# Performance work log

Hardware: AMD Instinct MI355X
Metric: run time of the kernel (lower is better)

The kernel has to match this reference:

```python
import jax, jax.numpy as jnp
import numpy as np
import math

GRID_SIZE = 5
ORDER = 3
TAU = 0.1            # HuxleyRD tau (constructor default)
Q_SCALE = 64 / 2.0   # SaturatedQuantizer levels=64


def make_grid():
    h = 2.0 / GRID_SIZE
    # knots: arange(-order, grid_size+order+1)*h - 1  -> 12 values, shared by all in_features
    return jnp.arange(-ORDER, GRID_SIZE + ORDER + 1, dtype=jnp.float32) * h - 1.0


def b_splines(x, grid):
    # x: [b, in] -> bases: [b, in, GRID_SIZE+ORDER] via vectorized Cox-de Boor
    xg = x[..., None]
    g = grid  # [12], identical per feature so plain broadcasting suffices
    bases = ((xg >= g[:-1]) & (xg < g[1:])).astype(x.dtype)  # [b, in, 11]
    for p in range(1, ORDER + 1):
        t_i, t_ip = g[:-1 - p], g[p:-1]
        term1 = (xg - t_i) / (t_ip - t_i + 1e-8) * bases[..., :-1]
        t_i1, t_ip1 = g[1:-p], g[p + 1:]
        term2 = (t_ip1 - xg) / (t_ip1 - t_i1 + 1e-8) * bases[..., 1:]
        bases = term1 + term2
    return bases  # [b, in, 8]


def kan_layer(x, base_w, spline_w, grid):
    base = x @ base_w.T
    basis = b_splines(x, grid)
    # SaturatedQuantizer forward (round to levels); STE expressed via stop_gradient
    qw = spline_w + jax.lax.stop_gradient(jnp.round(spline_w * Q_SCALE) / Q_SCALE - spline_w)
    return base + jnp.einsum('bic,oic->bo', basis, qw)


def trig_unfolding(u, gcve_pressure, chirality, tau_decay):
    # u: [b, n]
    tr_c = jnp.sum(u * u, axis=-1)                                   # [b]
    uf_abs = jnp.abs(jnp.fft.rfft(u, axis=-1))                       # [b, n//2+1]
    det_pas = jnp.var(uf_abs, axis=-1, ddof=1) + 1e-6                # torch.var is unbiased
    denom = 2.0 * jnp.sqrt(det_pas) ** 3 + 1e-8
    cos_3phi = jnp.clip((3.0 * gcve_pressure - tr_c / tau_decay) / denom, -0.999, 0.999)
    phi = jnp.arccos(cos_3phi) / 3.0                                 # [b]
    lam_min = jnp.min(uf_abs, axis=-1)                               # [b]
    amp = 2.0 * jnp.sqrt(lam_min / 3.0 + 1e-8)                       # [b]
    ks = jnp.arange(3, dtype=u.dtype)                                # branch indices 0,1,2
    cos_terms = jnp.cos(phi[None, :] + 2.0 * jnp.pi * ks[:, None] / 3.0)   # [3, b]
    shifts = jnp.exp(-jnp.abs(chirality)[None, :] * ks[:, None])           # [3, b]
    coef = amp[None, :] * cos_terms * shifts                                # [3, b]
    branches = coef[:, :, None] * u[None, :, :]                             # [3, b, n]
    energies = jnp.linalg.norm(branches, axis=-1)                           # [3, b]
    best_k = jnp.argmax(energies, axis=0)                                   # [b]
    mask = (best_k[None, :] == jnp.arange(3)[:, None]).astype(u.dtype)      # [3, b]
    return jnp.sum(branches * mask[:, :, None], axis=0)


def huxley_rd(u, spectral_gate, kernel, a, gamma, tau_decay, soliton_velocity,
              gcve_pressure, chirality):
    N = u.shape[-1]
    # HarmonicWaveDecomposition: spectral sigmoid gate split
    uf = jnp.fft.rfft(u, axis=-1)
    gate = jax.nn.sigmoid(spectral_gate)
    u_erg = jnp.fft.irfft(uf * gate, n=N, axis=-1)
    u_ne = jnp.fft.irfft(uf * (1.0 - gate), n=N, axis=-1)
    # ergodic: cubic reaction + 3-tap diffusion conv (padding=1, cross-correlation)
    reaction = u_erg * (u_erg - a) * (1.0 - u_erg)
    up = jnp.pad(u_erg, ((0, 0), (1, 1)))
    diffusion = kernel[0] * up[:, :-2] + kernel[1] * up[:, 1:-1] + kernel[2] * up[:, 2:]
    u_erg_next = u_erg + TAU * (reaction + gamma * diffusion)
    # non-ergodic: spectral phase shift (soliton translation)
    nef = jnp.fft.rfft(u_ne, axis=-1)
    k_idx = jnp.arange(nef.shape[-1], dtype=jnp.float32)
    phase = jnp.exp(-1j * 2.0 * jnp.pi * k_idx * soliton_velocity / N)
    u_ne_shift = jnp.fft.irfft(nef * phase, n=N, axis=-1)
    u_ne_unf = trig_unfolding(u_ne_shift, gcve_pressure, chirality, tau_decay)
    s = u_erg_next + u_ne_unf
    return jax.nn.sigmoid(s) * s  # SiLU-style fusion


def setup_inputs() -> dict:
    key = jax.random.key(0)
    ks = jax.random.split(key, 12)
    B, NIN, W, NOUT = 4096, 512, 1024, 1024
    return {
        'c': jax.random.uniform(ks[0], (B, NIN), jnp.float32, -1.0, 1.0),
        'base_w0': jax.random.normal(ks[1], (W, NIN), jnp.float32) * (1.0 / np.sqrt(NIN)),
        'spline_w0': jax.random.normal(ks[2], (W, NIN, 8), jnp.float32) * 0.1,
        'base_w1': jax.random.normal(ks[3], (W, W), jnp.float32) * (1.0 / np.sqrt(W)),
        'spline_w1': jax.random.normal(ks[4], (W, W, 8), jnp.float32) * 0.1,
        'base_w2': jax.random.normal(ks[5], (NOUT, W), jnp.float32) * (1.0 / np.sqrt(W)),
        'spline_w2': jax.random.normal(ks[6], (NOUT, W, 8), jnp.float32) * 0.1,
        'spectral_gate': jnp.ones((NOUT // 2 + 1,), jnp.float32),
        'diffusion_kernel': jnp.asarray([0.1, -0.2, 0.1], jnp.float32),
        'a_param': jnp.asarray(0.1, jnp.float32),
        'gamma': jnp.asarray(1.0, jnp.float32),
        'tau_decay': jnp.asarray(0.1, jnp.float32),
        'soliton_velocity': jnp.asarray(0.25, jnp.float32),
        'gcve_pressure': jax.random.uniform(ks[7], (B,), jnp.float32),
        'chirality': jax.random.normal(ks[8], (B,), jnp.float32),
    }


def reference(c, base_w0, spline_w0, base_w1, spline_w1, base_w2, spline_w2,
              spectral_gate, diffusion_kernel, a_param, gamma, tau_decay,
              soliton_velocity, gcve_pressure, chirality):
    grid = make_grid()
    x = kan_layer(c, base_w0, spline_w0, grid)
    x = kan_layer(x, base_w1, spline_w1, grid)
    x = kan_layer(x, base_w2, spline_w2, grid)
    return huxley_rd(x, spectral_gate, diffusion_kernel, a_param, gamma,
                     tau_decay, soliton_velocity, gcve_pressure, chirality)
```

## Files before the change

### kernel.cpp

```cpp
#include <hip/hip_runtime.h>
#include <math.h>

typedef _Float16 f16;
typedef _Float16 f16x8 __attribute__((ext_vector_type(8)));
typedef float f32x4 __attribute__((ext_vector_type(4)));

__global__ __launch_bounds__(256) void expand_sum_a(
    const float* __restrict__ src, size_t plane, int Sin,
    f16* __restrict__ Aexp, int KIN, int shift)
{
    int idx = blockIdx.x * 256 + threadIdx.x;
    int i = idx & (KIN - 1);
    int b = idx >> shift;
    float x = 0.0f;
    for (int s = 0; s < Sin; ++s) x += src[(size_t)s * plane + idx];

    float xs = (x + 2.2f) * 2.5f;
    float fj = floorf(xs);
    int jj = (int)fj;
    float t = xs - fj;
    float t2 = t * t, t3 = t2 * t;
    float omt = 1.0f - t;
    float p0 = omt * omt * omt * (1.0f / 6.0f);
    float p1 = (3.0f * t3 - 6.0f * t2 + 4.0f) * (1.0f / 6.0f);
    float p2 = (-3.0f * t3 + 3.0f * t2 + 3.0f * t + 1.0f) * (1.0f / 6.0f);
    float p3 = t3 * (1.0f / 6.0f);

    union { f16 h[8]; uint4 v; } hi, lo;
    bool inr = (jj >= 0 && jj <= 10);
    #pragma unroll
    for (int cc = 0; cc < 8; ++cc) {
        int d = cc - (jj - 3);
        float v = 0.0f;
        if (inr) {
            if (d == 0) v = p0; else if (d == 1) v = p1;
            else if (d == 2) v = p2; else if (d == 3) v = p3;
        }
        f16 h = (f16)v;
        hi.h[cc] = h;
        lo.h[cc] = (f16)(v - (float)h);
    }
    size_t KEXP = (size_t)KIN * 19;
    f16* row = Aexp + (size_t)b * KEXP;
    *(uint4*)(row + (size_t)i * 8) = hi.v;
    *(uint4*)(row + (size_t)KIN * 8 + (size_t)i * 8) = lo.v;
    f16 xh = (f16)x;
    f16 xl = (f16)(x - (float)xh);
    int K16 = KIN * 16;
    row[K16 + i] = xh;
    row[K16 + KIN + i] = xh;
    row[K16 + 2 * KIN + i] = xl;
}

__global__ __launch_bounds__(256) void prep_b(
    const float* __restrict__ BW, const float* __restrict__ SW,
    f16* __restrict__ Bexp, int KIN, int shift)
{
    int idx = blockIdx.x * 256 + threadIdx.x;
    int i = idx & (KIN - 1);
    int o = idx >> shift;
    const float* sp = SW + ((size_t)o * KIN + i) * 8;
    union { f16 h[8]; uint4 v; } pk;
    #pragma unroll
    for (int cc = 0; cc < 8; ++cc)
        pk.h[cc] = (f16)(rintf(sp[cc] * 32.0f) * 0.03125f);
    size_t KEXP = (size_t)KIN * 19;
    f16* row = Bexp + (size_t)o * KEXP;
    *(uint4*)(row + (size_t)i * 8) = pk.v;
    *(uint4*)(row + (size_t)KIN * 8 + (size_t)i * 8) = pk.v;
    float w = BW[(size_t)o * KIN + i];
    f16 wh = (f16)w;
    f16 wl = (f16)(w - (float)wh);
    int K16 = KIN * 16;
    row[K16 + i] = wh;
    row[K16 + KIN + i] = wl;
    row[K16 + 2 * KIN + i] = wh;
}

__global__ __launch_bounds__(512, 2) void gemm_mfma(
    const f16* __restrict__ A, const f16* __restrict__ Bm,
    float* __restrict__ C, int Kfull, int Kc, size_t plane, int N)
{
    __shared__ __align__(16) f16 As[4][8192];
    __shared__ __align__(16) f16 Bs[4][8192];

    const int tid = threadIdx.x;
    const int wave = tid >> 6, lane = tid & 63;

    const int nwg = gridDim.x * gridDim.y * gridDim.z;
    const int b = blockIdx.x + gridDim.x * (blockIdx.y + gridDim.y * blockIdx.z);
    const int q = nwg >> 3;
    const int L = (b & 7) * q + (b >> 3);
    const int lx = L % gridDim.x;
    const int rest = L / gridDim.x;
    const int ly = rest % gridDim.y;
    const int lz = rest / gridDim.y;

    const int m0 = ly * 256, n0 = lx * 256;
    const int kb = lz * Kc;
    int kcl = Kfull - kb; if (kcl > Kc) kcl = Kc;
    const int NT = kcl >> 5;

    const int kc_src = (lane & 3) ^ ((lane >> 3) & 3);
    const f16* gb[4];
    int isA_[4], coff[4];
    #pragma unroll
    for (int j = 0; j < 4; ++j) {
        int cch = wave * 4 + j;
        int a = (cch < 16);
        int c8 = a ? cch : (cch - 16);
        int row0 = (a ? m0 : n0) + c8 * 16 + (lane >> 2);
        gb[j] = (a ? A : Bm) + (size_t)row0 * Kfull + kb + kc_src * 8;
        isA_[j] = a;
        coff[j] = c8 * 512;
    }

    f32x4 acc[8][4];
    #pragma unroll
    for (int i = 0; i < 8; ++i)
        #pragma unroll
        for (int j = 0; j < 4; ++j)
            acc[i][j] = (f32x4){0.f, 0.f, 0.f, 0.f};

    #pragma unroll
    for (int s = 0; s < 3; ++s) {
        if (s < NT) {
            int k0 = s << 5;
            #pragma unroll
            for (int j = 0; j < 4; ++j) {
                f16* dp = isA_[j] ? &As[s][coff[j]] : &Bs[s][coff[j]];
                __builtin_amdgcn_global_load_lds(
                    (const __attribute__((address_space(1))) unsigned int*)(gb[j] + k0),
                    (__attribute__((address_space(3))) unsigned int*)dp, 16, 0, 0);
            }
        }
    }
    if (NT >= 3)      asm volatile("s_waitcnt vmcnt(8)" ::: "memory");
    else if (NT == 2) asm volatile("s_waitcnt vmcnt(4)" ::: "memory");
    else              asm volatile("s_waitcnt vmcnt(0)" ::: "memory");
    __builtin_amdgcn_s_barrier();
    asm volatile("" ::: "memory");

    const int lr = lane & 15;
    const int ko = (((lane >> 4) ^ ((lr >> 1) & 3)) & 3) * 8;
    const int wm = (wave & 1) * 128, wn = (wave >> 1) * 64;

    for (int t = 0; t < NT; ++t) {
        const int st = t & 3;
        const int ns = (t + 3) & 3;
        const bool pf = (t + 3 < NT);
        const int kn = (t + 3) << 5;
        const int rem = NT - 1 - t;

        f16x8 af[4], bf[4], ag[4];
        #pragma unroll
        for (int i = 0; i < 4; ++i)
            af[i] = *(const f16x8*)&As[st][(wm + i * 16 + lr) * 32 + ko];
        #pragma unroll
        for (int j = 0; j < 4; ++j)
            bf[j] = *(const f16x8*)&Bs[st][(wn + j * 16 + lr) * 32 + ko];
        if (pf) {
            #pragma unroll
            for (int j = 0; j < 2; ++j) {
                f16* dp = isA_[j] ? &As[ns][coff[j]] : &Bs[ns][coff[j]];
                __builtin_amdgcn_global_load_lds(
                    (const __attribute__((address_space(1))) unsigned int*)(gb[j] + kn),
                    (__attribute__((address_space(3))) unsigned int*)dp, 16, 0, 0);
            }
        }
        #pragma unroll
        for (int i = 0; i < 4; ++i)
            ag[i] = *(const f16x8*)&As[st][(wm + 64 + i * 16 + lr) * 32 + ko];
        if (pf) {
            #pragma unroll
            for (int j = 2; j < 4; ++j) {
                f16* dp = isA_[j] ? &As[ns][coff[j]] : &Bs[ns][coff[j]];
                __builtin_amdgcn_global_load_lds(
                    (const __attribute__((address_space(1))) unsigned int*)(gb[j] + kn),
                    (__attribute__((address_space(3))) unsigned int*)dp, 16, 0, 0);
            }
        }

        asm volatile("s_waitcnt lgkmcnt(4)" ::: "memory");
        __builtin_amdgcn_sched_barrier(0);
        __builtin_amdgcn_s_setprio(1);
        #pragma unroll
        for (int i = 0; i < 4; ++i)
            #pragma unroll
            for (int j = 0; j < 4; ++j)
                acc[i][j] = __builtin_amdgcn_mfma_f32_16x16x32_f16(af[i], bf[j], acc[i][j], 0, 0, 0);
        __builtin_amdgcn_s_setprio(0);

        asm volatile("s_waitcnt lgkmcnt(0)" ::: "memory");
        __builtin_amdgcn_sched_barrier(0);
        __builtin_amdgcn_s_setprio(1);
        #pragma unroll
        for (int i = 0; i < 4; ++i)
            #pragma unroll
            for (int j = 0; j < 4; ++j)
                acc[4 + i][j] = __builtin_amdgcn_mfma_f32_16x16x32_f16(ag[i], bf[j], acc[4 + i][j], 0, 0, 0);
        __builtin_amdgcn_s_setprio(0);

        if (rem >= 3)      asm volatile("s_waitcnt vmcnt(8)" ::: "memory");
        else if (rem == 2) asm volatile("s_waitcnt vmcnt(4)" ::: "memory");
        else if (rem == 1) asm volatile("s_waitcnt vmcnt(0)" ::: "memory");
        if (rem >= 1) {
            __builtin_amdgcn_sched_barrier(0);
            __builtin_amdgcn_s_barrier();
            asm volatile("" ::: "memory");
        }
    }

    float* Cp = C + (size_t)lz * plane;
    #pragma unroll
    for (int i = 0; i < 8; ++i) {
        int row = m0 + wm + i * 16 + (lane >> 4) * 4;
        #pragma unroll
        for (int j = 0; j < 4; ++j) {
            int col = n0 + wn + j * 16 + lr;
            #pragma unroll
            for (int rr = 0; rr < 4; ++rr)
                Cp[(size_t)(row + rr) * N + col] = acc[i][j][rr];
        }
    }
}

__global__ __launch_bounds__(256) void kan_gemm(
    const float* __restrict__ X, const float* __restrict__ BW,
    const float* __restrict__ SW, float* __restrict__ Y, int KIN, int OUT)
{
    __shared__ __align__(16) float Asf[72][68];
    __shared__ __align__(16) float Bsf[72][68];
    const int tid = threadIdx.x;
    const int n0 = blockIdx.x * 64;
    const int m0 = blockIdx.y * 64;
    const int tx = tid & 15;
    const int ty = tid >> 4;
    float acc[4][4] = {};
    for (int k0 = 0; k0 < KIN; k0 += 8) {
        #pragma unroll
        for (int rep = 0; rep < 2; ++rep) {
            int idx = rep * 256 + tid;
            int r = idx >> 3, c = idx & 7;
            float x = X[(size_t)(m0 + r) * KIN + k0 + c];
            int bk = c * 9;
            Asf[bk][r] = x;
            #pragma unroll
            for (int z = 0; z < 8; ++z) Asf[bk + 1 + z][r] = 0.0f;
            float xs = (x + 2.2f) * 2.5f;
            float fj = floorf(xs);
            int j = (int)fj;
            if (j >= 0 && j <= 10) {
                float t = xs - fj;
                float t2 = t * t, t3 = t2 * t;
                float omt = 1.0f - t;
                float p0 = omt * omt * omt * (1.0f / 6.0f);
                float p1 = (3.0f * t3 - 6.0f * t2 + 4.0f) * (1.0f / 6.0f);
                float p2 = (-3.0f * t3 + 3.0f * t2 + 3.0f * t + 1.0f) * (1.0f / 6.0f);
                float p3 = t3 * (1.0f / 6.0f);
                if (j >= 3) Asf[bk + 1 + j - 3][r] = p0;
                if (j >= 2 && j <= 9) Asf[bk + 1 + j - 2][r] = p1;
                if (j >= 1 && j <= 8) Asf[bk + 1 + j - 1][r] = p2;
                if (j <= 7) Asf[bk + 1 + j][r] = p3;
            }
        }
        #pragma unroll
        for (int rep = 0; rep < 16; ++rep) {
            int idx = rep * 256 + tid;
            int ol = idx >> 6;
            int l = idx & 63;
            int i = l >> 3, cc = l & 7;
            float v = SW[((size_t)(n0 + ol) * KIN + k0 + i) * 8 + cc];
            Bsf[i * 9 + 1 + cc][ol] = rintf(v * 32.0f) * 0.03125f;
        }
        #pragma unroll
        for (int rep = 0; rep < 2; ++rep) {
            int idx = rep * 256 + tid;
            int ol = idx >> 3, cc = idx & 7;
            Bsf[cc * 9][ol] = BW[(size_t)(n0 + ol) * KIN + k0 + cc];
        }
        __syncthreads();
        #pragma unroll 8
        for (int kk = 0; kk < 72; ++kk) {
            float4 av = *(const float4*)&Asf[kk][ty * 4];
            float4 bv = *(const float4*)&Bsf[kk][tx * 4];
            acc[0][0] += av.x * bv.x; acc[0][1] += av.x * bv.y; acc[0][2] += av.x * bv.z; acc[0][3] += av.x * bv.w;
            acc[1][0] += av.y * bv.x; acc[1][1] += av.y * bv.y; acc[1][2] += av.y * bv.z; acc[1][3] += av.y * bv.w;
            acc[2][0] += av.z * bv.x; acc[2][1] += av.z * bv.y; acc[2][2] += av.z * bv.z; acc[2][3] += av.z * bv.w;
            acc[3][0] += av.w * bv.x; acc[3][1] += av.w * bv.y; acc[3][2] += av.w * bv.z; acc[3][3] += av.w * bv.w;
        }
        __syncthreads();
    }
    #pragma unroll
    for (int i = 0; i < 4; ++i) {
        float4 o = make_float4(acc[i][0], acc[i][1], acc[i][2], acc[i][3]);
        *(float4*)&Y[(size_t)(m0 + ty * 4 + i) * OUT + n0 + tx * 4] = o;
    }
}

__device__ __forceinline__ float2 block_reduce_sum2(float2 v, float2* red, int tid) {
    red[tid] = v; __syncthreads();
    #pragma unroll
    for (int s = 128; s > 0; s >>= 1) {
        if (tid < s) {
            red[tid].x += red[tid + s].x;
            red[tid].y += red[tid + s].y;
        }
        __syncthreads();
    }
    float2 r = red[0]; __syncthreads();
    return r;
}
__device__ __forceinline__ float2 block_reduce_min2(float2 v, float2* red, int tid) {
    red[tid] = v; __syncthreads();
    #pragma unroll
    for (int s = 128; s > 0; s >>= 1) {
        if (tid < s) {
            red[tid].x = fminf(red[tid].x, red[tid + s].x);
            red[tid].y = fminf(red[tid].y, red[tid + s].y);
        }
        __syncthreads();
    }
    float2 r = red[0]; __syncthreads();
    return r;
}

__device__ void fft1024(float2* X, const float2* tw, int tid, bool inverse) {
    if (!inverse) {
        for (int sh = 9; sh >= 0; --sh) {
            int h = 1 << sh;
            #pragma unroll
            for (int q = 0; q < 2; ++q) {
                int b = tid + q * 256;
                int g = b >> sh, j = b & (h - 1);
                int i0 = (g << (sh + 1)) + j, i1 = i0 + h;
                float2 u = X[i0], v = X[i1];
                float dx = u.x - v.x, dy = u.y - v.y;
                X[i0] = make_float2(u.x + v.x, u.y + v.y);
                float2 w = tw[j << (9 - sh)];
                X[i1] = make_float2(dx * w.x + dy * w.y, dy * w.x - dx * w.y);
            }
            __syncthreads();
        }
    } else {
        for (int sh = 0; sh <= 9; ++sh) {
            int h = 1 << sh;
            #pragma unroll
            for (int q = 0; q < 2; ++q) {
                int b = tid + q * 256;
                int g = b >> sh, j = b & (h - 1);
                int i0 = (g << (sh + 1)) + j, i1 = i0 + h;
                float2 u = X[i0], v = X[i1];
                float2 w = tw[j << (9 - sh)];
                float tx2 = v.x * w.x - v.y * w.y;
                float ty2 = v.x * w.y + v.y * w.x;
                X[i0] = make_float2(u.x + tx2, u.y + ty2);
                X[i1] = make_float2(u.x - tx2, u.y - ty2);
            }
            __syncthreads();
        }
    }
}

__global__ __launch_bounds__(256) void huxley_kernel(
    const float* __restrict__ Pin, size_t plane, int S,
    float* __restrict__ dst,
    const float* __restrict__ sg, const float* __restrict__ dk,
    const float* __restrict__ pa, const float* __restrict__ pgam,
    const float* __restrict__ ptau, const float* __restrict__ pvel,
    const float* __restrict__ gp, const float* __restrict__ chi)
{
    __shared__ float2 A[1024];
    __shared__ float2 Bb[1024];
    __shared__ float2 sErg[1024];
    __shared__ float sAbs1[516];
    __shared__ float sAbs2[516];
    __shared__ float2 tw[512];
    __shared__ float2 red2[256];
    __shared__ float sG[516];

    const int tid = threadIdx.x;
    const int r0 = blockIdx.x * 2;
    const float* pin0 = Pin + (size_t)r0 * 1024;
    const float* pin1 = Pin + (size_t)(r0 + 1) * 1024;
    float* uo0 = dst + (size_t)r0 * 1024;
    float* uo1 = dst + (size_t)(r0 + 1) * 1024;

    for (int m = tid; m < 512; m += 256) {
        float s, c;
        sincosf(6.283185307179586f * (float)m * (1.0f / 1024.0f), &s, &c);
        tw[m] = make_float2(c, s);
    }
    for (int k = tid; k < 513; k += 256)
        sG[k] = 1.0f / (1.0f + expf(-sg[k]));
    for (int i = tid; i < 1024; i += 256) {
        float s0 = 0.0f, s1 = 0.0f;
        for (int ss = 0; ss < S; ++ss) {
            s0 += pin0[(size_t)ss * plane + i];
            s1 += pin1[(size_t)ss * plane + i];
        }
        A[i] = make_float2(s0, s1);
    }
    __syncthreads();

    fft1024(A, tw, tid, false);

    for (int p = tid; p < 1024; p += 256) {
        int k = (int)(__brev((unsigned)p) >> 22);
        int m = (k <= 512) ? k : 1024 - k;
        float g = sG[m] * (1.0f / 1024.0f);
        Bb[p] = make_float2(A[p].x * g, A[p].y * g);
    }
    __syncthreads();
    fft1024(Bb, tw, tid, true);
    for (int i = tid; i < 1024; i += 256) sErg[i] = Bb[i];
    __syncthreads();

    const float vv = pvel[0];
    for (int p = tid; p < 1024; p += 256) {
        int k = (int)(__brev((unsigned)p) >> 22);
        int m = (k <= 512) ? k : 1024 - k;
        float omg = 1.0f - sG[m];
        float2 z = A[p];
        float nx = z.x * omg, ny = z.y * omg;
        float ang = (k <= 512)
            ? (-6.283185307179586f * vv * (float)k * (1.0f / 1024.0f))
            : (6.283185307179586f * vv * (float)(1024 - k) * (1.0f / 1024.0f));
        float sn, cs;
        sincosf(ang, &sn, &cs);
        float yx, yy;
        if (k == 512) {
            yx = nx * cs;
            yy = ny * cs;
            sAbs1[512] = fabsf(nx * cs);
            sAbs2[512] = fabsf(ny * cs);
        } else {
            yx = nx * cs - ny * sn;
            yy = nx * sn + ny * cs;
            if (k < 512) {
                int p2 = (int)(__brev((unsigned)((1024 - k) & 1023)) >> 22);
                float2 z2 = A[p2];
                float f1x = 0.5f * (z.x + z2.x), f1y = 0.5f * (z.y - z2.y);
                float f2x = 0.5f * (z.y + z2.y), f2y = 0.5f * (z2.x - z.x);
                sAbs1[k] = omg * sqrtf(f1x * f1x + f1y * f1y);
                sAbs2[k] = omg * sqrtf(f2x * f2x + f2y * f2y);
            }
        }
        Bb[p] = make_float2(yx * (1.0f / 1024.0f), yy * (1.0f / 1024.0f));
    }
    __syncthreads();
    fft1024(Bb, tw, tid, true);

    float2 loc = make_float2(0.0f, 0.0f);
    for (int i = tid; i < 1024; i += 256) {
        loc.x += Bb[i].x * Bb[i].x;
        loc.y += Bb[i].y * Bb[i].y;
    }
    float2 trc = block_reduce_sum2(loc, red2, tid);

    loc = make_float2(0.0f, 0.0f);
    for (int k = tid; k < 513; k += 256) { loc.x += sAbs1[k]; loc.y += sAbs2[k]; }
    float2 msum = block_reduce_sum2(loc, red2, tid);
    float2 mean = make_float2(msum.x * (1.0f / 513.0f), msum.y * (1.0f / 513.0f));

    loc = make_float2(0.0f, 0.0f);
    for (int k = tid; k < 513; k += 256) {
        float d1 = sAbs1[k] - mean.x;
        float d2 = sAbs2[k] - mean.y;
        loc.x += d1 * d1; loc.y += d2 * d2;
    }
    float2 varsum = block_reduce_sum2(loc, red2, tid);

    loc = make_float2(3.4e38f, 3.4e38f);
    for (int k = tid; k < 513; k += 256) {
        loc.x = fminf(loc.x, sAbs1[k]);
        loc.y = fminf(loc.y, sAbs2[k]);
    }
    float2 lmin = block_reduce_min2(loc, red2, tid);

    const float tauv = ptau[0];
    float trcv[2]  = { trc.x, trc.y };
    float varv[2]  = { varsum.x, varsum.y };
    float lminv[2] = { lmin.x, lmin.y };
    float gpv[2]   = { gp[r0], gp[r0 + 1] };
    float chv[2]   = { chi[r0], chi[r0 + 1] };
    float cb[2];
    #pragma unroll
    for (int rr = 0; rr < 2; ++rr) {
        float det_pas = varv[rr] * (1.0f / 512.0f) + 1e-6f;
        float sd = sqrtf(det_pas);
        float denom = 2.0f * sd * sd * sd + 1e-8f;
        float c3 = (3.0f * gpv[rr] - trcv[rr] / tauv) / denom;
        c3 = fminf(fmaxf(c3, -0.999f), 0.999f);
        float ph = acosf(c3) * (1.0f / 3.0f);
        float amp = 2.0f * sqrtf(lminv[rr] * (1.0f / 3.0f) + 1e-8f);
        float nu = sqrtf(trcv[rr]);
        float achi = fabsf(chv[rr]);
        float cbest = 0.0f, ebest = -1.0f;
        #pragma unroll
        for (int kb = 0; kb < 3; ++kb) {
            float ck = amp * cosf(ph + 2.0943951023931953f * (float)kb) * expf(-achi * (float)kb);
            float ek = fabsf(ck) * nu;
            if (ek > ebest) { ebest = ek; cbest = ck; }
        }
        cb[rr] = cbest;
    }

    const float a = pa[0], gm = pgam[0];
    const float k0 = dk[0], k1 = dk[1], k2 = dk[2];
    for (int i = tid; i < 1024; i += 256) {
        float2 e = sErg[i];
        float2 l = (i > 0) ? sErg[i - 1] : make_float2(0.0f, 0.0f);
        float2 r = (i < 1023) ? sErg[i + 1] : make_float2(0.0f, 0.0f);
        float reac1 = e.x * (e.x - a) * (1.0f - e.x);
        float diff1 = k0 * l.x + k1 * e.x + k2 * r.x;
        float un1 = e.x + 0.1f * (reac1 + gm * diff1);
        float s1 = un1 + cb[0] * Bb[i].x;
        uo0[i] = s1 / (1.0f + expf(-s1));
        float reac2 = e.y * (e.y - a) * (1.0f - e.y);
        float diff2 = k0 * l.y + k1 * e.y + k2 * r.y;
        float un2 = e.y + 0.1f * (reac2 + gm * diff2);
        float s2 = un2 + cb[1] * Bb[i].y;
        uo1[i] = s2 / (1.0f + expf(-s2));
    }
}


extern "C" void kernel_launch(void* const* d_in, const int* in_sizes, int n_in,
                              void* d_out, int out_size, void* d_ws, size_t ws_size,
                              hipStream_t stream) {
    const float* c    = (const float*)d_in[0];
    const float* bw0  = (const float*)d_in[1];
    const float* sw0  = (const float*)d_in[2];
    const float* bw1  = (const float*)d_in[3];
    const float* sw1  = (const float*)d_in[4];
    const float* bw2  = (const float*)d_in[5];
    const float* sw2  = (const float*)d_in[6];
    const float* sg   = (const float*)d_in[7];
    const float* dk   = (const float*)d_in[8];
    const float* pa   = (const float*)d_in[9];
    const float* pgam = (const float*)d_in[10];
    const float* ptau = (const float*)d_in[11];
    const float* pvel = (const float*)d_in[12];
    const float* gp   = (const float*)d_in[13];
    const float* chi  = (const float*)d_in[14];

    const int B = 4096, NIN = 512, W = 1024, NOUT = 1024;
    const int KE0 = 19 * NIN, KE1 = 19 * W;
    const size_t MN = (size_t)B * W;
    const size_t BE = (size_t)W * KE1 * 2;
    dim3 blk(256);
    dim3 gblk(512);

    struct Cand { int CH, S; };
    const Cand cands[] = {
        {4096, 4}, {4096, 3}, {2048, 4}, {2048, 3}, {1024, 4},
        {512, 4}, {256, 4}
    };
    int CH = 0, S = 1;
    for (const auto& cd : cands) {
        size_t need = BE + (size_t)cd.CH * KE1 * 2 + (size_t)cd.S * MN * 4;
        if (need <= ws_size) { CH = cd.CH; S = cd.S; break; }
    }

    if (CH > 0) {
        f16* Bexp = (f16*)d_ws;
        float* P  = (float*)((char*)d_ws + BE);
        f16* Aexp = (f16*)((char*)d_ws + BE + (size_t)S * MN * 4);

        const int Kc0 = ((KE0 / 32 + S - 1) / S) * 32;
        const int Kc1 = ((KE1 / 32 + S - 1) / S) * 32;

        prep_b<<<(W * NIN) / 256, blk, 0, stream>>>(bw0, sw0, Bexp, NIN, 9);
        for (int r0 = 0; r0 < B; r0 += CH) {
            expand_sum_a<<<(CH * NIN) / 256, blk, 0, stream>>>(
                c + (size_t)r0 * NIN, 0, 1, Aexp, NIN, 9);
            gemm_mfma<<<dim3(W / 256, CH / 256, S), gblk, 0, stream>>>(
                Aexp, Bexp, P + (size_t)r0 * W, KE0, Kc0, MN, W);
        }
        prep_b<<<(W * W) / 256, blk, 0, stream>>>(bw1, sw1, Bexp, W, 10);
        for (int r0 = 0; r0 < B; r0 += CH) {
            expand_sum_a<<<(CH * W) / 256, blk, 0, stream>>>(
                P + (size_t)r0 * W, MN, S, Aexp, W, 10);
            gemm_mfma<<<dim3(W / 256, CH / 256, S), gblk, 0, stream>>>(
                Aexp, Bexp, P + (size_t)r0 * W, KE1, Kc1, MN, W);
        }
        prep_b<<<(NOUT * W) / 256, blk, 0, stream>>>(bw2, sw2, Bexp, W, 10);
        for (int r0 = 0; r0 < B; r0 += CH) {
            expand_sum_a<<<(CH * W) / 256, blk, 0, stream>>>(
                P + (size_t)r0 * W, MN, S, Aexp, W, 10);
            gemm_mfma<<<dim3(NOUT / 256, CH / 256, S), gblk, 0, stream>>>(
                Aexp, Bexp, P + (size_t)r0 * W, KE1, Kc1, MN, NOUT);
        }
        huxley_kernel<<<B / 2, blk, 0, stream>>>(P, MN, S, (float*)d_out,
                                                 sg, dk, pa, pgam, ptau, pvel, gp, chi);
    } else {
        float* fx0 = (float*)d_ws;
        float* fx1 = fx0 + (size_t)B * W;
        dim3 g0(W / 64, B / 64);
        kan_gemm<<<g0, blk, 0, stream>>>(c,   bw0, sw0, fx0, NIN, W);
        kan_gemm<<<g0, blk, 0, stream>>>(fx0, bw1, sw1, fx1, W,   W);
        dim3 g2(NOUT / 64, B / 64);
        kan_gemm<<<g2, blk, 0, stream>>>(fx1, bw2, sw2, (float*)d_out, W, NOUT);
        huxley_kernel<<<B / 2, blk, 0, stream>>>((float*)d_out, 0, 1, (float*)d_out,
                                                 sg, dk, pa, pgam, ptau, pvel, gp, chi);
    }
}
```

Before: 670.5 us.

## Add double-buffered GEMM variant with split-K of eight and higher occupancy

Adds a gemm_mfma2 kernel that uses two LDS stages instead of a deeper pipeline, which cuts shared memory so that four 512-thread workgroups can be resident per CU (launch_bounds 512,4). It adds a split-K=8 candidate that selects this kernel when the workspace is large enough, giving more workgroups to fill the GPU. The cost is more partial-sum planes to write and then reduce in expand_sum_a and the huxley kernel, plus shallower prefetch per workgroup.

Result: no change. 665.0 us (median of 2 runs) (-0.8%).

```diff
diff --git a/kernel.cpp b/kernel.cpp
--- a/kernel.cpp
+++ b/kernel.cpp
@@ -205,6 +205,143 @@
         else if (rem == 2) asm volatile("s_waitcnt vmcnt(4)" ::: "memory");
         else if (rem == 1) asm volatile("s_waitcnt vmcnt(0)" ::: "memory");
         if (rem >= 1) {
+            __builtin_amdgcn_sched_barrier(0);
+            __builtin_amdgcn_s_barrier();
+            asm volatile("" ::: "memory");
+        }
+    }
+
+    float* Cp = C + (size_t)lz * plane;
+    #pragma unroll
+    for (int i = 0; i < 8; ++i) {
+        int row = m0 + wm + i * 16 + (lane >> 4) * 4;
+        #pragma unroll
+        for (int j = 0; j < 4; ++j) {
+            int col = n0 + wn + j * 16 + lr;
+            #pragma unroll
+            for (int rr = 0; rr < 4; ++rr)
+                Cp[(size_t)(row + rr) * N + col] = acc[i][j][rr];
+        }
+    }
+}
+
+__global__ __launch_bounds__(512, 4) void gemm_mfma2(
+    const f16* __restrict__ A, const f16* __restrict__ Bm,
+    float* __restrict__ C, int Kfull, int Kc, size_t plane, int N)
+{
+    __shared__ __align__(16) f16 As[2][8192];
+    __shared__ __align__(16) f16 Bs[2][8192];
+
+    const int tid = threadIdx.x;
+    const int wave = tid >> 6, lane = tid & 63;
+
+    const int nwg = gridDim.x * gridDim.y * gridDim.z;
+    const int b = blockIdx.x + gridDim.x * (blockIdx.y + gridDim.y * blockIdx.z);
+    const int q = nwg >> 3;
+    const int L = (b & 7) * q + (b >> 3);
+    const int lx = L % gridDim.x;
+    const int rest = L / gridDim.x;
+    const int ly = rest % gridDim.y;
+    const int lz = rest / gridDim.y;
+
+    const int m0 = ly * 256, n0 = lx * 256;
+    const int kb = lz * Kc;
+    int kcl = Kfull - kb; if (kcl > Kc) kcl = Kc;
+    const int NT = kcl >> 5;
+
+    const int kc_src = (lane & 3) ^ ((lane >> 3) & 3);
+    const f16* gb[4];
+    int isA_[4], coff[4];
+    #pragma unroll
+    for (int j = 0; j < 4; ++j) {
+        int cch = wave * 4 + j;
+        int a = (cch < 16);
+        int c8 = a ? cch : (cch - 16);
+        int row0 = (a ? m0 : n0) + c8 * 16 + (lane >> 2);
+        gb[j] = (a ? A : Bm) + (size_t)row0 * Kfull + kb + kc_src * 8;
+        isA_[j] = a;
+        coff[j] = c8 * 512;
+    }
+
+    f32x4 acc[8][4];
+    #pragma unroll
+    for (int i = 0; i < 8; ++i)
+        #pragma unroll
+        for (int j = 0; j < 4; ++j)
+            acc[i][j] = (f32x4){0.f, 0.f, 0.f, 0.f};
+
+    #pragma unroll
+    for (int j = 0; j < 4; ++j) {
+        f16* dp = isA_[j] ? &As[0][coff[j]] : &Bs[0][coff[j]];
+        __builtin_amdgcn_global_load_lds(
+            (const __attribute__((address_space(1))) unsigned int*)(gb[j]),
+            (__attribute__((address_space(3))) unsigned int*)dp, 16, 0, 0);
+    }
+    asm volatile("s_waitcnt vmcnt(0)" ::: "memory");
+    __builtin_amdgcn_s_barrier();
+    asm volatile("" ::: "memory");
+
+    const int lr = lane & 15;
+    const int ko = (((lane >> 4) ^ ((lr >> 1) & 3)) & 3) * 8;
+    const int wm = (wave & 1) * 128, wn = (wave >> 1) * 64;
+
+    for (int t = 0; t < NT; ++t) {
+        const int st = t & 1;
+        const int ns = st ^ 1;
+        const bool pf = (t + 1 < NT);
+        const int kn = (t + 1) << 5;
+
+        f16x8 af[4], bf[4], ag[4];
+        #pragma unroll
+        for (int i = 0; i < 4; ++i)
+            af[i] = *(const f16x8*)&As[st][(wm + i * 16 + lr) * 32 + ko];
+        #pragma unroll
+        for (int j = 0; j < 4; ++j)
+            bf[j] = *(const f16x8*)&Bs[st][(wn + j * 16 + lr) * 32 + ko];
+        if (pf) {
+            #pragma unroll
+            for (int j = 0; j < 2; ++j) {
+                f16* dp = isA_[j] ? &As[ns][coff[j]] : &Bs[ns][coff[j]];
+                __builtin_amdgcn_global_load_lds(
+                    (const __attribute__((address_space(1))) unsigned int*)(gb[j] + kn),
+                    (__attribute__((address_space(3))) unsigned int*)dp, 16, 0, 0);
+            }
+        }
+        #pragma unroll
+        for (int i = 0; i < 4; ++i)
+            ag[i] = *(const f16x8*)&As[st][(wm + 64 + i * 16 + lr) * 32 + ko];
+        if (pf) {
+            #pragma unroll
+            for (int j = 2; j < 4; ++j) {
+                f16* dp = isA_[j] ? &As[ns][coff[j]] : &Bs[ns][coff[j]];
+                __builtin_amdgcn_global_load_lds(
+                    (const __attribute__((address_space(1))) unsigned int*)(gb[j] + kn),
+                    (__attribute__((address_space(3))) unsigned int*)dp, 16, 0, 0);
+            }
+        }
+
+        asm volatile("s_waitcnt lgkmcnt(4)" ::: "memory");
+        __builtin_amdgcn_sched_barrier(0);
+        __builtin_amdgcn_s_setprio(1);
+        #pragma unroll
+        for (int i = 0; i < 4; ++i)
+            #pragma unroll
+            for (int j = 0; j < 4; ++j)
+                acc[i][j] = __builtin_amdgcn_mfma_f32_16x16x32_f16(af[i], bf[j], acc[i][j], 0, 0, 0);
+        __builtin_amdgcn_s_setprio(0);
+
+        asm volatile("s_waitcnt lgkmcnt(0)" ::: "memory");
+        __builtin_amdgcn_sched_barrier(0);
+        __builtin_amdgcn_s_setprio(1);
+        #pragma unroll
+        for (int i = 0; i < 4; ++i)
+            #pragma unroll
+            for (int j = 0; j < 4; ++j)
+                acc[4 + i][j] = __builtin_amdgcn_mfma_f32_16x16x32_f16(ag[i], bf[j], acc[4 + i][j], 0, 0, 0);
+        __builtin_amdgcn_s_setprio(0);
+
+        if (pf) {
+            asm volatile("s_waitcnt vmcnt(0)" ::: "memory");
             __builtin_amdgcn_sched_barrier(0);
             __builtin_amdgcn_s_barrier();
             asm volatile("" ::: "memory");
@@ -554,6 +691,7 @@
 
     struct Cand { int CH, S; };
     const Cand cands[] = {
+        {4096, 8},
         {4096, 4}, {4096, 3}, {2048, 4}, {2048, 3}, {1024, 4},
         {512, 4}, {256, 4}
     };
@@ -567,6 +705,7 @@
         f16* Bexp = (f16*)d_ws;
         float* P  = (float*)((char*)d_ws + BE);
         f16* Aexp = (f16*)((char*)d_ws + BE + (size_t)S * MN * 4);
+        const bool deep = (S == 8);
 
         const int Kc0 = ((KE0 / 32 + S - 1) / S) * 32;
         const int Kc1 = ((KE1 / 32 + S - 1) / S) * 32;
@@ -575,22 +714,34 @@
         for (int r0 = 0; r0 < B; r0 += CH) {
             expand_sum_a<<<(CH * NIN) / 256, blk, 0, stream>>>(
                 c + (size_t)r0 * NIN, 0, 1, Aexp, NIN, 9);
-            gemm_mfma<<<dim3(W / 256, CH / 256, S), gblk, 0, stream>>>(
-                Aexp, Bexp, P + (size_t)r0 * W, KE0, Kc0, MN, W);
+            if (deep)
+                gemm_mfma2<<<dim3(W / 256, CH / 256, S), gblk, 0, stream>>>(
+                    Aexp, Bexp, P + (size_t)r0 * W, KE0, Kc0, MN, W);
+            else
+                gemm_mfma<<<dim3(W / 256, CH / 256, S), gblk, 0, stream>>>(
+                    Aexp, Bexp, P + (size_t)r0 * W, KE0, Kc0, MN, W);
         }
         prep_b<<<(W * W) / 256, blk, 0, stream>>>(bw1, sw1, Bexp, W, 10);
         for (int r0 = 0; r0 < B; r0 += CH) {
             expand_sum_a<<<(CH * W) / 256, blk, 0, stream>>>(
                 P + (size_t)r0 * W, MN, S, Aexp, W, 10);
-            gemm_mfma<<<dim3(W / 256, CH / 256, S), gblk, 0, stream>>>(
-                Aexp, Bexp, P + (size_t)r0 * W, KE1, Kc1, MN, W);
+            if (deep)
+                gemm_mfma2<<<dim3(W / 256, CH / 256, S), gblk, 0, stream>>>(
+                    Aexp, Bexp, P + (size_t)r0 * W, KE1, Kc1, MN, W);
+            else
+                gemm_mfma<<<dim3(W / 256, CH / 256, S), gblk, 0, stream>>>(
+                    Aexp, Bexp, P + (size_t)r0 * W, KE1, Kc1, MN, W);
         }
         prep_b<<<(NOUT * W) / 256, blk, 0, stream>>>(bw2, sw2, Bexp, W, 10);
         for (int r0 = 0; r0 < B; r0 += CH) {
             expand_sum_a<<<(CH * W) / 256, blk, 0, stream>>>(
                 P + (size_t)r0 * W, MN, S, Aexp, W, 10);
-            gemm_mfma<<<dim3(NOUT / 256, CH / 256, S), gblk, 0, stream>>>(
-                Aexp, Bexp, P + (size_t)r0 * W, KE1, Kc1, MN, NOUT);
+            if (deep)
+                gemm_mfma2<<<dim3(NOUT / 256, CH / 256, S), gblk, 0, stream>>>(
+                    Aexp, Bexp, P + (size_t)r0 * W, KE1, Kc1, MN, NOUT);
+            else
+                gemm_mfma<<<dim3(NOUT / 256, CH / 256, S), gblk, 0, stream>>>(
+                    Aexp, Bexp, P + (size_t)r0 * W, KE1, Kc1, MN, NOUT);
         }
         huxley_kernel<<<B / 2, blk, 0, stream>>>(P, MN, S, (float*)d_out,
                                                  sg, dk, pa, pgam, ptau, pvel, gp, chi);
```

## Shrink MFMA GEMM tile to 128x128 with 256 threads and double buffering

Applied to the files above, without the earlier changes.

The f16 MFMA GEMM moves from 256x256 tiles with 512 threads and a 4-stage LDS pipeline to 128x128 tiles with 256 threads and 2-stage double buffering. Each wave now holds a 4x4 block of 16x16 accumulators, and launch bounds allow 4 blocks per CU. The aim is more workgroups, better occupancy and less LDS per block. The cost is lower arithmetic intensity per tile, more global traffic, and shallower prefetch that may expose load latency.

Result: slower. 799.5 us (+19.2%).

```diff
diff --git a/kernel.cpp b/kernel.cpp
--- a/kernel.cpp
+++ b/kernel.cpp
@@ -77,12 +77,12 @@
     row[K16 + 2 * KIN + i] = wh;
 }
 
-__global__ __launch_bounds__(512, 2) void gemm_mfma(
+__global__ __launch_bounds__(256, 4) void gemm_mfma(
     const f16* __restrict__ A, const f16* __restrict__ Bm,
     float* __restrict__ C, int Kfull, int Kc, size_t plane, int N)
 {
-    __shared__ __align__(16) f16 As[4][8192];
-    __shared__ __align__(16) f16 Bs[4][8192];
+    __shared__ __align__(16) f16 As[2][4096];
+    __shared__ __align__(16) f16 Bs[2][4096];
 
     const int tid = threadIdx.x;
     const int wave = tid >> 6, lane = tid & 63;
@@ -96,7 +96,7 @@
     const int ly = rest % gridDim.y;
     const int lz = rest / gridDim.y;
 
-    const int m0 = ly * 256, n0 = lx * 256;
+    const int m0 = ly * 128, n0 = lx * 128;
     const int kb = lz * Kc;
     int kcl = Kfull - kb; if (kcl > Kc) kcl = Kc;
     const int NT = kcl >> 5;
@@ -107,85 +107,69 @@
     #pragma unroll
     for (int j = 0; j < 4; ++j) {
         int cch = wave * 4 + j;
-        int a = (cch < 16);
-        int c8 = a ? cch : (cch - 16);
+        int a = (cch < 8);
+        int c8 = a ? cch : (cch - 8);
         int row0 = (a ? m0 : n0) + c8 * 16 + (lane >> 2);
         gb[j] = (a ? A : Bm) + (size_t)row0 * Kfull + kb + kc_src * 8;
         isA_[j] = a;
         coff[j] = c8 * 512;
     }
 
-    f32x4 acc[8][4];
-    #pragma unroll
-    for (int i = 0; i < 8; ++i)
+    f32x4 acc[4][4];
+    #pragma unroll
+    for (int i = 0; i < 4; ++i)
         #pragma unroll
         for (int j = 0; j < 4; ++j)
             acc[i][j] = (f32x4){0.f, 0.f, 0.f, 0.f};
 
     #pragma unroll
-    for (int s = 0; s < 3; ++s) {
-        if (s < NT) {
-            int k0 = s << 5;
-            #pragma unroll
-            for (int j = 0; j < 4; ++j) {
-                f16* dp = isA_[j] ? &As[s][coff[j]] : &Bs[s][coff[j]];
-                __builtin_amdgcn_global_load_lds(
-                    (const __attribute__((address_space(1))) unsigned int*)(gb[j] + k0),
-                    (__attribute__((address_space(3))) unsigned int*)dp, 16, 0, 0);
-            }
-        }
-    }
-    if (NT >= 3)      asm volatile("s_waitcnt vmcnt(8)" ::: "memory");
-    else if (NT == 2) asm volatile("s_waitcnt vmcnt(4)" ::: "memory");
-    else              asm volatile("s_waitcnt vmcnt(0)" ::: "memory");
+    for (int j = 0; j < 4; ++j) {
+        f16* dp = isA_[j] ? &As[0][coff[j]] : &Bs[0][coff[j]];
+        __builtin_amdgcn_global_load_lds(
+            (const __attribute__((address_space(1))) unsigned int*)(gb[j]),
+            (__attribute__((address_space(3))) unsigned int*)dp, 16, 0, 0);
+    }
+    asm volatile("s_waitcnt vmcnt(0)" ::: "memory");
     __builtin_amdgcn_s_barrier();
     asm volatile("" ::: "memory");
 
     const int lr = lane & 15;
     const int ko = (((lane >> 4) ^ ((lr >> 1) & 3)) & 3) * 8;
-    const int wm = (wave & 1) * 128, wn = (wave >> 1) * 64;
+    const int wm = (wave >> 1) * 64, wn = (wave & 1) * 64;
 
     for (int t = 0; t < NT; ++t) {
-        const int st = t & 3;
-        const int ns = (t + 3) & 3;
-        const bool pf = (t + 3 < NT);
-        const int kn = (t + 3) << 5;
-        const int rem = NT - 1 - t;
-
-        f16x8 af[4], bf[4], ag[4];
-        #pragma unroll
-        for (int i = 0; i < 4; ++i)
+        const int st = t & 1;
+        const int ns = st ^ 1;
+        const bool pf = (t + 1 < NT);
+        const int kn = (t + 1) << 5;
+
+        f16x8 af[4], bf[4];
+        #pragma unroll
+        for (int i = 0; i < 2; ++i)
             af[i] = *(const f16x8*)&As[st][(wm + i * 16 + lr) * 32 + ko];
         #pragma unroll
         for (int j = 0; j < 4; ++j)
             bf[j] = *(const f16x8*)&Bs[st][(wn + j * 16 + lr) * 32 + ko];
+        __builtin_amdgcn_sched_barrier(0);
+        #pragma unroll
+        for (int i = 2; i < 4; ++i)
+            af[i] = *(const f16x8*)&As[st][(wm + i * 16 + lr) * 32 + ko];
+        __builtin_amdgcn_sched_barrier(0);
         if (pf) {
             #pragma unroll
-            for (int j = 0; j < 2; ++j) {
+            for (int j = 0; j < 4; ++j) {
                 f16* dp = isA_[j] ? &As[ns][coff[j]] : &Bs[ns][coff[j]];
                 __builtin_amdgcn_global_load_lds(
                     (const __attribute__((address_space(1))) unsigned int*)(gb[j] + kn),
                     (__attribute__((address_space(3))) unsigned int*)dp, 16, 0, 0);
             }
         }
-        #pragma unroll
-        for (int i = 0; i < 4; ++i)
-            ag[i] = *(const f16x8*)&As[st][(wm + 64 + i * 16 + lr) * 32 + ko];
-        if (pf) {
-            #pragma unroll
-            for (int j = 2; j < 4; ++j) {
-                f16* dp = isA_[j] ? &As[ns][coff[j]] : &Bs[ns][coff[j]];
-                __builtin_amdgcn_global_load_lds(
-                    (const __attribute__((address_space(1))) unsigned int*)(gb[j] + kn),
-                    (__attribute__((address_space(3))) unsigned int*)dp, 16, 0, 0);
-            }
-        }
-
-        asm volatile("s_waitcnt lgkmcnt(4)" ::: "memory");
+
+        asm volatile("s_waitcnt lgkmcnt(2)" ::: "memory");
         __builtin_amdgcn_sched_barrier(0);
         __builtin_amdgcn_s_setprio(1);
         #pragma unroll
-        for (int i = 0; i < 4; ++i)
+        for (int i = 0; i < 2; ++i)
             #pragma unroll
             for (int j = 0; j < 4; ++j)
                 acc[i][j] = __builtin_amdgcn_mfma_f32_16x16x32_f16(af[i], bf[j], acc[i][j], 0, 0, 0);
@@ -195,16 +179,14 @@
         __builtin_amdgcn_sched_barrier(0);
         __builtin_amdgcn_s_setprio(1);
         #pragma unroll
-        for (int i = 0; i < 4; ++i)
+        for (int i = 2; i < 4; ++i)
             #pragma unroll
             for (int j = 0; j < 4; ++j)
-                acc[4 + i][j] = __builtin_amdgcn_mfma_f32_16x16x32_f16(ag[i], bf[j], acc[4 + i][j], 0, 0, 0);
+                acc[i][j] = __builtin_amdgcn_mfma_f32_16x16x32_f16(af[i], bf[j], acc[i][j], 0, 0, 0);
         __builtin_amdgcn_s_setprio(0);
 
-        if (rem >= 3)      asm volatile("s_waitcnt vmcnt(8)" ::: "memory");
-        else if (rem == 2) asm volatile("s_waitcnt vmcnt(4)" ::: "memory");
-        else if (rem == 1) asm volatile("s_waitcnt vmcnt(0)" ::: "memory");
-        if (rem >= 1) {
+        if (pf) {
+            asm volatile("s_waitcnt vmcnt(0)" ::: "memory");
             __builtin_amdgcn_sched_barrier(0);
             __builtin_amdgcn_s_barrier();
             asm volatile("" ::: "memory");
@@ -213,7 +195,7 @@
 
     float* Cp = C + (size_t)lz * plane;
     #pragma unroll
-    for (int i = 0; i < 8; ++i) {
+    for (int i = 0; i < 4; ++i) {
         int row = m0 + wm + i * 16 + (lane >> 4) * 4;
         #pragma unroll
         for (int j = 0; j < 4; ++j) {
@@ -550,7 +532,6 @@
     const size_t MN = (size_t)B * W;
     const size_t BE = (size_t)W * KE1 * 2;
     dim3 blk(256);
-    dim3 gblk(512);
 
     struct Cand { int CH, S; };
     const Cand cands[] = {
@@ -575,21 +556,21 @@
         for (int r0 = 0; r0 < B; r0 += CH) {
             expand_sum_a<<<(CH * NIN) / 256, blk, 0, stream>>>(
                 c + (size_t)r0 * NIN, 0, 1, Aexp, NIN, 9);
-            gemm_mfma<<<dim3(W / 256, CH / 256, S), gblk, 0, stream>>>(
+            gemm_mfma<<<dim3(W / 128, CH / 128, S), blk, 0, stream>>>(
                 Aexp, Bexp, P + (size_t)r0 * W, KE0, Kc0, MN, W);
         }
         prep_b<<<(W * W) / 256, blk, 0, stream>>>(bw1, sw1, Bexp, W, 10);
         for (int r0 = 0; r0 < B; r0 += CH) {
             expand_sum_a<<<(CH * W) / 256, blk, 0, stream>>>(
                 P + (size_t)r0 * W, MN, S, Aexp, W, 10);
-            gemm_mfma<<<dim3(W / 256, CH / 256, S), gblk, 0, stream>>>(
+            gemm_mfma<<<dim3(W / 128, CH / 128, S), blk, 0, stream>>>(
                 Aexp, Bexp, P + (size_t)r0 * W, KE1, Kc1, MN, W);
         }
         prep_b<<<(NOUT * W) / 256, blk, 0, stream>>>(bw2, sw2, Bexp, W, 10);
         for (int r0 = 0; r0 < B; r0 += CH) {
             expand_sum_a<<<(CH * W) / 256, blk, 0, stream>>>(
                 P + (size_t)r0 * W, MN, S, Aexp, W, 10);
-            gemm_mfma<<<dim3(NOUT / 256, CH / 256, S), gblk, 0, stream>>>(
+            gemm_mfma<<<dim3(NOUT / 128, CH / 128, S), blk, 0, stream>>>(
                 Aexp, Bexp, P + (size_t)r0 * W, KE1, Kc1, MN, NOUT);
         }
         huxley_kernel<<<B / 2, blk, 0, stream>>>(P, MN, S, (float*)d_out,
```

## Restructure MFMA GEMM to BK=64 double-buffered half-tile pipeline

Applied to the files above, without the earlier changes.

Reworks the main fp16 MFMA GEMM from a 4-stage BK=32 pipeline to a 2-buffer BK=64 scheme. Each buffer is split into A and B halves, and loads are interleaved between four MFMA quadrants. The LDS swizzle is widened to 8 chunks for 64-wide rows, and the K-chunk split is rounded to multiples of 64. The aim is fewer barriers per unit of work and better overlap of global-to-LDS loads with MFMA. The cost is a shallower prefetch depth, which could expose memory latency.

Measured after the change: 681.3 us. Within noise of the previous version (+1.6%).

```diff
diff --git a/kernel.cpp b/kernel.cpp
--- a/kernel.cpp
+++ b/kernel.cpp
@@ -77,6 +77,10 @@
     row[K16 + 2 * KIN + i] = wh;
 }
 
+#define GLD16(dst, src) __builtin_amdgcn_global_load_lds( \
+    (const __attribute__((address_space(1))) unsigned int*)(src), \
+    (__attribute__((address_space(3))) unsigned int*)(dst), 16, 0, 0)
+
 __global__ __launch_bounds__(512, 2) void gemm_mfma(
     const f16* __restrict__ A, const f16* __restrict__ Bm,
     float* __restrict__ C, int Kfull, int Kc, size_t plane, int N)
@@ -99,21 +103,32 @@
     const int m0 = ly * 256, n0 = lx * 256;
     const int kb = lz * Kc;
     int kcl = Kfull - kb; if (kcl > Kc) kcl = Kc;
-    const int NT = kcl >> 5;
-
-    const int kc_src = (lane & 3) ^ ((lane >> 3) & 3);
-    const f16* gb[4];
-    int isA_[4], coff[4];
-    #pragma unroll
-    for (int j = 0; j < 4; ++j) {
-        int cch = wave * 4 + j;
-        int a = (cch < 16);
-        int c8 = a ? cch : (cch - 16);
-        int row0 = (a ? m0 : n0) + c8 * 16 + (lane >> 2);
-        gb[j] = (a ? A : Bm) + (size_t)row0 * Kfull + kb + kc_src * 8;
-        isA_[j] = a;
-        coff[j] = c8 * 512;
-    }
+    const int NT = kcl >> 6;
+
+    const int l3 = lane >> 3;
+    const int kc_src = ((lane & 7) ^ l3);
+    const f16* pA[2][2];
+    const f16* pB[2][2];
+    #pragma unroll
+    for (int h = 0; h < 2; ++h) {
+        #pragma unroll
+        for (int j = 0; j < 2; ++j) {
+            int g = wave * 2 + j;
+            int rA = g * 8 + l3 + h * 64 + ((g >= 8) ? 64 : 0);
+            int cB = (g * 8 & 31) + l3 + (g >> 2) * 64 + h * 32;
+            pA[h][j] = A  + (size_t)(m0 + rA) * Kfull + kb + kc_src * 8;
+            pB[h][j] = Bm + (size_t)(n0 + cB) * Kfull + kb + kc_src * 8;
+        }
+    }
+    const int dst0 = (wave * 2) * 512 + lane * 8;
+    const int dst1 = (wave * 2 + 1) * 512 + lane * 8;
+
+    #define STAGE_A(buf, h, koff) do { \
+        GLD16(&As[(buf)*2+(h)][dst0], pA[h][0] + (koff)); \
+        GLD16(&As[(buf)*2+(h)][dst1], pA[h][1] + (koff)); } while (0)
+    #define STAGE_B(buf, h, koff) do { \
+        GLD16(&Bs[(buf)*2+(h)][dst0], pB[h][0] + (koff)); \
+        GLD16(&Bs[(buf)*2+(h)][dst1], pB[h][1] + (koff)); } while (0)
 
     f32x4 acc[8][4];
     #pragma unroll
@@ -122,89 +137,112 @@
         for (int j = 0; j < 4; ++j)
             acc[i][j] = (f32x4){0.f, 0.f, 0.f, 0.f};
 
-    #pragma unroll
-    for (int s = 0; s < 3; ++s) {
-        if (s < NT) {
-            int k0 = s << 5;
-            #pragma unroll
-            for (int j = 0; j < 4; ++j) {
-                f16* dp = isA_[j] ? &As[s][coff[j]] : &Bs[s][coff[j]];
-                __builtin_amdgcn_global_load_lds(
-                    (const __attribute__((address_space(1))) unsigned int*)(gb[j] + k0),
-                    (__attribute__((address_space(3))) unsigned int*)dp, 16, 0, 0);
-            }
-        }
-    }
-    if (NT >= 3)      asm volatile("s_waitcnt vmcnt(8)" ::: "memory");
-    else if (NT == 2) asm volatile("s_waitcnt vmcnt(4)" ::: "memory");
-    else              asm volatile("s_waitcnt vmcnt(0)" ::: "memory");
+    STAGE_A(0, 0, 0);
+    STAGE_B(0, 0, 0);
+    STAGE_B(0, 1, 0);
+    STAGE_A(0, 1, 0);
+    asm volatile("s_waitcnt vmcnt(4)" ::: "memory");
     __builtin_amdgcn_s_barrier();
     asm volatile("" ::: "memory");
 
     const int lr = lane & 15;
-    const int ko = (((lane >> 4) ^ ((lr >> 1) & 3)) & 3) * 8;
+    const int g4 = lane >> 4;
+    const int swz = lr & 7;
+    const int ko0 = ((g4)     ^ swz) * 8;
+    const int ko1 = ((4 + g4) ^ swz) * 8;
+    const int aid = (wave & 1) * 64;
+    const int bid = (wave >> 1) * 32;
     const int wm = (wave & 1) * 128, wn = (wave >> 1) * 64;
 
+    f16x8 afr[4][2], bfr[2][2][2];
+
     for (int t = 0; t < NT; ++t) {
-        const int st = t & 3;
-        const int ns = (t + 3) & 3;
-        const bool pf = (t + 3 < NT);
-        const int kn = (t + 3) << 5;
-        const int rem = NT - 1 - t;
-
-        f16x8 af[4], bf[4], ag[4];
-        #pragma unroll
-        for (int i = 0; i < 4; ++i)
-            af[i] = *(const f16x8*)&As[st][(wm + i * 16 + lr) * 32 + ko];
-        #pragma unroll
-        for (int j = 0; j < 4; ++j)
-            bf[j] = *(const f16x8*)&Bs[st][(wn + j * 16 + lr) * 32 + ko];
+        const int rb = t & 1, wb = rb ^ 1;
+        const bool pf = (t + 1 < NT);
+        const int kt = (t + 1) << 6;
+
+        #pragma unroll
+        for (int mf = 0; mf < 4; ++mf) {
+            afr[mf][0] = *(const f16x8*)&As[rb * 2 + 0][(aid + mf * 16 + lr) * 64 + ko0];
+            afr[mf][1] = *(const f16x8*)&As[rb * 2 + 0][(aid + mf * 16 + lr) * 64 + ko1];
+        }
+        #pragma unroll
+        for (int nf = 0; nf < 2; ++nf) {
+            bfr[0][nf][0] = *(const f16x8*)&Bs[rb * 2 + 0][(bid + nf * 16 + lr) * 64 + ko0];
+            bfr[0][nf][1] = *(const f16x8*)&Bs[rb * 2 + 0][(bid + nf * 16 + lr) * 64 + ko1];
+        }
+        __builtin_amdgcn_sched_barrier(0);
+        if (pf) STAGE_A(wb, 0, kt);
+        if (pf) asm volatile("s_waitcnt vmcnt(4)" ::: "memory");
+        else    asm volatile("s_waitcnt vmcnt(2)" ::: "memory");
+        __builtin_amdgcn_sched_barrier(0);
+        __builtin_amdgcn_s_barrier();
+        asm volatile("s_waitcnt lgkmcnt(0)" ::: "memory");
+        __builtin_amdgcn_sched_barrier(0);
+        __builtin_amdgcn_s_setprio(1);
+        #pragma unroll
+        for (int mf = 0; mf < 4; ++mf)
+            #pragma unroll
+            for (int nf = 0; nf < 2; ++nf) {
+                acc[mf][nf] = __builtin_amdgcn_mfma_f32_16x16x32_f16(afr[mf][0], bfr[0][nf][0], acc[mf][nf], 0, 0, 0);
+                acc[mf][nf] = __builtin_amdgcn_mfma_f32_16x16x32_f16(afr[mf][1], bfr[0][nf][1], acc[mf][nf], 0, 0, 0);
+            }
+        __builtin_amdgcn_s_setprio(0);
+
+        #pragma unroll
+        for (int nf = 0; nf < 2; ++nf) {
+            bfr[1][nf][0] = *(const f16x8*)&Bs[rb * 2 + 1][(bid + nf * 16 + lr) * 64 + ko0];
+            bfr[1][nf][1] = *(const f16x8*)&Bs[rb * 2 + 1][(bid + nf * 16 + lr) * 64 + ko1];
+        }
+        __builtin_amdgcn_sched_barrier(0);
+        if (pf) STAGE_B(wb, 0, kt);
+        if (pf) asm volatile("s_waitcnt vmcnt(4)" ::: "memory");
+        else    asm volatile("s_waitcnt vmcnt(0)" ::: "memory");
+        __builtin_amdgcn_sched_barrier(0);
+        __builtin_amdgcn_s_barrier();
+        asm volatile("s_waitcnt lgkmcnt(0)" ::: "memory");
+        __builtin_amdgcn_sched_barrier(0);
+        __builtin_amdgcn_s_setprio(1);
+        #pragma unroll
+        for (int mf = 0; mf < 4; ++mf)
+            #pragma unroll
+            for (int nf = 0; nf < 2; ++nf) {
+                acc[mf][2 + nf] = __builtin_amdgcn_mfma_f32_16x16x32_f16(afr[mf][0], bfr[1][nf][0], acc[mf][2 + nf], 0, 0, 0);
+                acc[mf][2 + nf] = __builtin_amdgcn_mfma_f32_16x16x32_f16(afr[mf][1], bfr[1][nf][1], acc[mf][2 + nf], 0, 0, 0);
+            }
+        __builtin_amdgcn_s_setprio(0);
+
+        #pragma unroll
+        for (int mf = 0; mf < 4; ++mf) {
+            afr[mf][0] = *(const f16x8*)&As[rb * 2 + 1][(aid + mf * 16 + lr) * 64 + ko0];
+            afr[mf][1] = *(const f16x8*)&As[rb * 2 + 1][(aid + mf * 16 + lr) * 64 + ko1];
+        }
+        __builtin_amdgcn_sched_barrier(0);
+        if (pf) STAGE_B(wb, 1, kt);
+        asm volatile("s_waitcnt lgkmcnt(0)" ::: "memory");
+        __builtin_amdgcn_sched_barrier(0);
+        __builtin_amdgcn_s_setprio(1);
+        #pragma unroll
+        for (int mf = 0; mf < 4; ++mf)
+            #pragma unroll
+            for (int nf = 0; nf < 2; ++nf) {
+                acc[4 + mf][nf] = __builtin_amdgcn_mfma_f32_16x16x32_f16(afr[mf][0], bfr[0][nf][0], acc[4 + mf][nf], 0, 0, 0);
+                acc[4 + mf][nf] = __builtin_amdgcn_mfma_f32_16x16x32_f16(afr[mf][1], bfr[0][nf][1], acc[4 + mf][nf], 0, 0, 0);
+            }
+        __builtin_amdgcn_s_setprio(0);
+
+        __builtin_amdgcn_s_setprio(1);
+        #pragma unroll
+        for (int mf = 0; mf < 4; ++mf)
+            #pragma unroll
+            for (int nf = 0; nf < 2; ++nf) {
+                acc[4 + mf][2 + nf] = __builtin_amdgcn_mfma_f32_16x16x32_f16(afr[mf][0], bfr[1][nf][0], acc[4 + mf][2 + nf], 0, 0, 0);
+                acc[4 + mf][2 + nf] = __builtin_amdgcn_mfma_f32_16x16x32_f16(afr[mf][1], bfr[1][nf][1], acc[4 + mf][2 + nf], 0, 0, 0);
+            }
+        __builtin_amdgcn_s_setprio(0);
         if (pf) {
-            #pragma unroll
-            for (int j = 0; j < 2; ++j) {
-                f16* dp = isA_[j] ? &As[ns][coff[j]] : &Bs[ns][coff[j]];
-                __builtin_amdgcn_global_load_lds(
-                    (const __attribute__((address_space(1))) unsigned int*)(gb[j] + kn),
-                    (__attribute__((address_space(3))) unsigned int*)dp, 16, 0, 0);
-            }
-        }
-        #pragma unroll
-        for (int i = 0; i < 4; ++i)
-            ag[i] = *(const f16x8*)&As[st][(wm + 64 + i * 16 + lr) * 32 + ko];
-        if (pf) {
-            #pragma unroll
-            for (int j = 2; j < 4; ++j) {
-                f16* dp = isA_[j] ? &As[ns][coff[j]] : &Bs[ns][coff[j]];
-                __builtin_amdgcn_global_load_lds(
-                    (const __attribute__((address_space(1))) unsigned int*)(gb[j] + kn),
-                    (__attribute__((address_space(3))) unsigned int*)dp, 16, 0, 0);
-            }
-        }
-
-        asm volatile("s_waitcnt lgkmcnt(4)" ::: "memory");
-        __builtin_amdgcn_sched_barrier(0);
-        __builtin_amdgcn_s_setprio(1);
-        #pragma unroll
-        for (int i = 0; i < 4; ++i)
-            #pragma unroll
-            for (int j = 0; j < 4; ++j)
-                acc[i][j] = __builtin_amdgcn_mfma_f32_16x16x32_f16(af[i], bf[j], acc[i][j], 0, 0, 0);
-        __builtin_amdgcn_s_setprio(0);
-
-        asm volatile("s_waitcnt lgkmcnt(0)" ::: "memory");
-        __builtin_amdgcn_sched_barrier(0);
-        __builtin_amdgcn_s_setprio(1);
-        #pragma unroll
-        for (int i = 0; i < 4; ++i)
-            #pragma unroll
-            for (int j = 0; j < 4; ++j)
-                acc[4 + i][j] = __builtin_amdgcn_mfma_f32_16x16x32_f16(ag[i], bf[j], acc[4 + i][j], 0, 0, 0);
-        __builtin_amdgcn_s_setprio(0);
-
-        if (rem >= 3)      asm volatile("s_waitcnt vmcnt(8)" ::: "memory");
-        else if (rem == 2) asm volatile("s_waitcnt vmcnt(4)" ::: "memory");
-        else if (rem == 1) asm volatile("s_waitcnt vmcnt(0)" ::: "memory");
-        if (rem >= 1) {
+            STAGE_A(wb, 1, kt);
+            asm volatile("s_waitcnt vmcnt(4)" ::: "memory");
             __builtin_amdgcn_sched_barrier(0);
             __builtin_amdgcn_s_barrier();
             asm volatile("" ::: "memory");
@@ -223,6 +261,8 @@
                 Cp[(size_t)(row + rr) * N + col] = acc[i][j][rr];
         }
     }
+    #undef STAGE_A
+    #undef STAGE_B
 }
 
 __global__ __launch_bounds__(256) void kan_gemm(
@@ -568,8 +608,8 @@
         float* P  = (float*)((char*)d_ws + BE);
         f16* Aexp = (f16*)((char*)d_ws + BE + (size_t)S * MN * 4);
 
-        const int Kc0 = ((KE0 / 32 + S - 1) / S) * 32;
-        const int Kc1 = ((KE1 / 32 + S - 1) / S) * 32;
+        const int Kc0 = ((KE0 / 64 + S - 1) / S) * 64;
+        const int Kc1 = ((KE1 / 64 + S - 1) / S) * 64;
 
         prep_b<<<(W * NIN) / 256, blk, 0, stream>>>(bw0, sw0, Bexp, NIN, 9);
         for (int r0 = 0; r0 < B; r0 += CH) {
```
